# Performance work log

Hardware: AMD Instinct MI355X
Metric: run time of the kernel (lower is better)

## Reference

```python
import jax, jax.numpy as jnp
import numpy as np

B, S, H = 2, 2048, 1024
NH, HD = 16, 64
SCALE = HD ** -0.5


def setup_inputs() -> dict:
    key = jax.random.key(0)
    k1, k2, k3, k4 = jax.random.split(key, 4)
    hidden_states = jax.random.normal(k1, (B, S, H), dtype=jnp.float32)
    attention_mask = jax.random.randint(k2, (B, S), 0, 2, dtype=jnp.int32)
    # xavier-uniform-ish init scale
    w_qkv = jax.random.normal(k3, (3 * H, H), dtype=jnp.float32) * (2.0 / (H + 3 * H)) ** 0.5
    w_out = jax.random.normal(k4, (H, H), dtype=jnp.float32) * (1.0 / H) ** 0.5
    return {"hidden_states": hidden_states, "attention_mask": attention_mask,
            "w_qkv": w_qkv, "w_out": w_out}


def reference(hidden_states, attention_mask, w_qkv, w_out):
    b, s, _ = hidden_states.shape
    qkv = hidden_states @ w_qkv.T                      # [B,S,3H]
    q, k, v = jnp.split(qkv, 3, axis=-1)
    # [B,S,H] -> [B,NH,S,HD]
    reshape = lambda x: x.reshape(b, s, NH, HD).transpose(0, 2, 1, 3)
    q, k, v = reshape(q), reshape(k), reshape(v)
    scores = jnp.einsum('bhqd,bhkd->bhqk', q, k) * SCALE   # [B,NH,S,S]
    mask = attention_mask[:, None, None, :] == 0           # [B,1,1,S]
    scores = jnp.where(mask, -jnp.inf, scores)
    attn = jax.nn.softmax(scores, axis=-1)                 # dropout p: eval mode -> identity
    out = jnp.einsum('bhqk,bhkd->bhqd', attn, v)           # [B,NH,S,HD]
    out = out.transpose(0, 2, 1, 3).reshape(b, s, H)
    return out @ w_out.T
```

## Files before the change

kernel.cpp:

```cpp
#include <hip/hip_runtime.h>
#include <string.h>


typedef __bf16    bf16x8 __attribute__((ext_vector_type(8)));
typedef _Float16  f16x4  __attribute__((ext_vector_type(4)));
typedef _Float16  f16x2  __attribute__((ext_vector_type(2)));
typedef float     f32x4  __attribute__((ext_vector_type(4)));

#define NTOK   4096
#define HDIM   1024
#define SEQ    2048
#define NHEAD  16
#define F2SHIFT 4.0f
#define QSCALE  0.18033688f
#define LSTRIDE 68

__device__ __forceinline__ float bf2f(unsigned short u) {
    union { unsigned int i; float f; } x;
    x.i = ((unsigned int)u) << 16;
    return x.f;
}
__device__ __forceinline__ unsigned short f2bf(float f) {
    union { __bf16 h; unsigned short u; } x;
    x.h = (__bf16)f;
    return x.u;
}
__device__ __forceinline__ unsigned short f2h(float f) {
    union { _Float16 h; unsigned short u; } x;
    x.h = (_Float16)f;
    return x.u;
}
__device__ __forceinline__ f16x2 pkrtz(float a, float b) {
    union { __fp16 __attribute__((ext_vector_type(2))) i; f16x2 o; } x;
    x.i = __builtin_amdgcn_cvt_pkrtz(a, b);
    return x.o;
}

__device__ __forceinline__ int detect_f32(const unsigned short* hs) {
    unsigned int idx = (threadIdx.x & 63) * 4096u;
    float f = bf2f(hs[idx]);
    return __any(!(fabsf(f) < 1e4f));
}

typedef const __attribute__((address_space(1))) unsigned int* gptr_u32;
typedef __attribute__((address_space(3))) unsigned int* lptr_u32;

__device__ __forceinline__ void async16(const unsigned short* g, unsigned short* l) {
    __builtin_amdgcn_global_load_lds((gptr_u32)g, (lptr_u32)l, 16, 0, 0);
}

__global__ void convert3_kernel(const void* __restrict__ s0, const void* __restrict__ s1,
                                const void* __restrict__ s2, unsigned short* __restrict__ dst) {
    const int isf32 = detect_f32((const unsigned short*)s0);
    if (!isf32) return;
    int g = blockIdx.x * blockDim.x + threadIdx.x;
    const int stride = gridDim.x * blockDim.x;
    for (; g < 1048576; g += stride) {
        int i = g * 8;
        const void* src; int off;
        if (i < 4194304)      { src = s0; off = i; }
        else if (i < 7340032) { src = s1; off = i - 4194304; }
        else                  { src = s2; off = i - 7340032; }
        const float* s = (const float*)src + off;
        unsigned short o[8];
#pragma unroll
        for (int j = 0; j < 8; j++) o[j] = f2bf(s[j]);
        *(uint4*)(dst + i) = *(const uint4*)o;
    }
}

__global__ __launch_bounds__(256) void gemm_qkv(
    const unsigned short* __restrict__ Xc, const unsigned short* __restrict__ Wc,
    const unsigned short* __restrict__ Xraw, const unsigned short* __restrict__ Wraw,
    unsigned short* __restrict__ q_out, unsigned short* __restrict__ k_out,
    unsigned short* __restrict__ v_out) {
    const int K = 1024;
    __shared__ __align__(16) unsigned short Xs[128 * 32];
    __shared__ __align__(16) unsigned short Ws[128 * 32];

    const int isf32 = detect_f32(Xraw);
    const unsigned short* X = isf32 ? Xc : Xraw;
    const unsigned short* W = isf32 ? Wc : Wraw;

    const int t = threadIdx.x;
    const int w = t >> 6, lane = t & 63, quad = lane >> 4, lr = lane & 15;
    const int wrow = (w >> 1) * 64, wcol = (w & 1) * 64;
    const int m0 = blockIdx.y * 128, n0 = blockIdx.x * 128;
    const bool vblk = (n0 >= 2048);

    f32x4 acc[4][4];
#pragma unroll
    for (int mi = 0; mi < 4; mi++)
#pragma unroll
        for (int ni = 0; ni < 4; ni++) acc[mi][ni] = (f32x4){0.f, 0.f, 0.f, 0.f};

    const int srow = w * 32 + (lane >> 2);
    const int scol = (lane & 3) * 8;
    const unsigned short* xg = X + (size_t)(m0 + srow) * K + scol;
    const unsigned short* wg = W + (size_t)(n0 + srow) * K + scol;
    unsigned short* xl0 = &Xs[w * 1024];
    unsigned short* wl0 = &Ws[w * 1024];

    for (int k0 = 0; k0 < K; k0 += 32) {
        __syncthreads();
        async16(xg + k0, xl0);
        async16(xg + k0 + 16 * K, xl0 + 512);
        async16(wg + k0, wl0);
        async16(wg + k0 + 16 * K, wl0 + 512);
        __syncthreads();
        bf16x8 af[4], bfr[4];
#pragma unroll
        for (int mi = 0; mi < 4; mi++)
            af[mi] = *(bf16x8*)&Xs[(wrow + mi * 16 + lr) * 32 + quad * 8];
#pragma unroll
        for (int ni = 0; ni < 4; ni++)
            bfr[ni] = *(bf16x8*)&Ws[(wcol + ni * 16 + lr) * 32 + quad * 8];
        if (!vblk) {
#pragma unroll
            for (int mi = 0; mi < 4; mi++)
#pragma unroll
                for (int ni = 0; ni < 4; ni++)
                    acc[mi][ni] = __builtin_amdgcn_mfma_f32_16x16x32_bf16(af[mi], bfr[ni], acc[mi][ni], 0, 0, 0);
        } else {
#pragma unroll
            for (int mi = 0; mi < 4; mi++)
#pragma unroll
                for (int ni = 0; ni < 4; ni++)
                    acc[mi][ni] = __builtin_amdgcn_mfma_f32_16x16x32_bf16(bfr[ni], af[mi], acc[mi][ni], 0, 0, 0);
        }
    }

    if (!vblk) {
#pragma unroll
        for (int mi = 0; mi < 4; mi++)
#pragma unroll
            for (int ni = 0; ni < 4; ni++)
#pragma unroll
                for (int rr = 0; rr < 4; rr++) {
                    int mrow = m0 + wrow + mi * 16 + quad * 4 + rr;
                    int j = n0 + wcol + ni * 16 + lr;
                    float val = acc[mi][ni][rr];
                    int which = j >> 10, rem = j & 1023;
                    int nh = rem >> 6, hd = rem & 63;
                    int b = mrow >> 11, s = mrow & 2047;
                    size_t dst = ((size_t)(b * NHEAD + nh) * SEQ + s) * 64 + hd;
                    if (which == 0) q_out[dst] = f2bf(val * QSCALE);
                    else            k_out[dst] = f2bf(val);
                }
    } else {
#pragma unroll
        for (int mi = 0; mi < 4; mi++)
#pragma unroll
            for (int ni = 0; ni < 4; ni++)
#pragma unroll
                for (int rr = 0; rr < 4; rr++) {
                    int n = n0 + wcol + ni * 16 + quad * 4 + rr;
                    int m = m0 + wrow + mi * 16 + lr;
                    float val = acc[mi][ni][rr];
                    int rem = n & 1023;
                    int nh = rem >> 6, hd = rem & 63;
                    int b = m >> 11, s = m & 2047;
                    size_t dst = ((size_t)(b * NHEAD + nh) * 64 + hd) * SEQ + s;
                    v_out[dst] = f2h(val);
                }
    }
}

__global__ __launch_bounds__(256) void gemm_out(
    const unsigned short* __restrict__ X, const unsigned short* __restrict__ Wc,
    const unsigned short* __restrict__ Wraw,
    void* __restrict__ d_out, const unsigned short* __restrict__ hs_raw) {
    const int K = 1024, N = 1024;
    __shared__ __align__(16) unsigned short Xs[64 * 32];
    __shared__ __align__(16) unsigned short Ws[128 * 32];

    const int isf32 = detect_f32(hs_raw);
    const unsigned short* W = isf32 ? Wc : Wraw;

    const int t = threadIdx.x;
    const int w = t >> 6, lane = t & 63, quad = lane >> 4, lr = lane & 15;
    const int wrow = (w >> 1) * 32, wcol = (w & 1) * 64;
    const int m0 = blockIdx.y * 64, n0 = blockIdx.x * 128;

    f32x4 acc[2][4];
#pragma unroll
    for (int mi = 0; mi < 2; mi++)
#pragma unroll
        for (int ni = 0; ni < 4; ni++) acc[mi][ni] = (f32x4){0.f, 0.f, 0.f, 0.f};

    const int sxrow = w * 16 + (lane >> 2);
    const int swrow = w * 32 + (lane >> 2);
    const int scol = (lane & 3) * 8;
    const unsigned short* xg = X + (size_t)(m0 + sxrow) * K + scol;
    const unsigned short* wg = W + (size_t)(n0 + swrow) * K + scol;
    unsigned short* xl0 = &Xs[w * 512];
    unsigned short* wl0 = &Ws[w * 1024];

    for (int k0 = 0; k0 < K; k0 += 32) {
        __syncthreads();
        async16(xg + k0, xl0);
        async16(wg + k0, wl0);
        async16(wg + k0 + 16 * K, wl0 + 512);
        __syncthreads();
        bf16x8 af[2], bfr[4];
#pragma unroll
        for (int mi = 0; mi < 2; mi++)
            af[mi] = *(bf16x8*)&Xs[(wrow + mi * 16 + lr) * 32 + quad * 8];
#pragma unroll
        for (int ni = 0; ni < 4; ni++)
            bfr[ni] = *(bf16x8*)&Ws[(wcol + ni * 16 + lr) * 32 + quad * 8];
#pragma unroll
        for (int mi = 0; mi < 2; mi++)
#pragma unroll
            for (int ni = 0; ni < 4; ni++)
                acc[mi][ni] = __builtin_amdgcn_mfma_f32_16x16x32_bf16(af[mi], bfr[ni], acc[mi][ni], 0, 0, 0);
    }

#pragma unroll
    for (int mi = 0; mi < 2; mi++)
#pragma unroll
        for (int ni = 0; ni < 4; ni++)
#pragma unroll
            for (int rr = 0; rr < 4; rr++) {
                int mrow = m0 + wrow + mi * 16 + quad * 4 + rr;
                int j = n0 + wcol + ni * 16 + lr;
                float val = acc[mi][ni][rr];
                size_t dst = (size_t)mrow * N + j;
                if (isf32) ((float*)d_out)[dst] = val;
                else ((unsigned short*)d_out)[dst] = f2bf(val);
            }
}

__global__ __launch_bounds__(256) void flash_attn_v7(
    const unsigned short* __restrict__ q, const unsigned short* __restrict__ k,
    const unsigned short* __restrict__ vt, const int* __restrict__ mask,
    unsigned short* __restrict__ attn_out) {
    __shared__ __align__(16) unsigned short Ks[64 * LSTRIDE];
    __shared__ __align__(16) unsigned short Vt[64 * LSTRIDE];
    __shared__ __align__(16) float Msk[80];

    const int t = threadIdx.x;
    const int w = t >> 6, lane = t & 63, quad = lane >> 4, lr = lane & 15;
    const int bh = blockIdx.x, b = bh >> 4, h = bh & 15;
    const int q0 = blockIdx.y * 128;

    const unsigned short* qb = q + (size_t)bh * SEQ * 64;
    const unsigned short* kb = k + (size_t)bh * SEQ * 64;
    const unsigned short* vtb = vt + (size_t)bh * 64 * SEQ;
    const int* mb = mask + b * SEQ;

    bf16x8 qf[2][2];
#pragma unroll
    for (int qg = 0; qg < 2; qg++) {
        const unsigned short* qrow = qb + (size_t)(q0 + w * 32 + qg * 16 + lr) * 64 + quad * 8;
        qf[qg][0] = *(const bf16x8*)qrow;
        qf[qg][1] = *(const bf16x8*)(qrow + 32);
    }

    f32x4 oacc[2][4];
#pragma unroll
    for (int qg = 0; qg < 2; qg++)
#pragma unroll
        for (int dt = 0; dt < 4; dt++) oacc[qg][dt] = (f32x4){0.f, 0.f, 0.f, 0.f};
    float l_st[2] = {0.f, 0.f};

    const int sr = t >> 2;
    const int sc = (t & 3) * 16;

    for (int kk0 = 0; kk0 < SEQ; kk0 += 64) {
        const uint4* kp = (const uint4*)(kb + (size_t)(kk0 + sr) * 64 + sc);
        const uint4* vp = (const uint4*)(vtb + (size_t)sr * SEQ + kk0 + sc);
        uint4 ka = kp[0], kb2 = kp[1];
        uint4 va = vp[0], vb2 = vp[1];
        float mval = 0.f;
        if (t < 64) mval = (mb[kk0 + t] == 0) ? -1e30f : -F2SHIFT;

        __syncthreads();
        *(uint4*)&Ks[sr * LSTRIDE + sc] = ka;
        *(uint4*)&Ks[sr * LSTRIDE + sc + 8] = kb2;
        *(uint4*)&Vt[sr * LSTRIDE + sc] = va;
        *(uint4*)&Vt[sr * LSTRIDE + sc + 8] = vb2;
        if (t < 64) Msk[t] = mval;
        __syncthreads();

#pragma unroll
        for (int mt = 0; mt < 4; mt++) {
            bf16x8 a1h0 = *(bf16x8*)&Ks[(mt * 16 + lr) * LSTRIDE + quad * 8];
            bf16x8 a1h1 = *(bf16x8*)&Ks[(mt * 16 + lr) * LSTRIDE + 32 + quad * 8];
            f16x4 a2[4];
#pragma unroll
            for (int dt = 0; dt < 4; dt++)
                a2[dt] = *(f16x4*)&Vt[(dt * 16 + lr) * LSTRIDE + mt * 16 + quad * 4];
            float4 mv = *(const float4*)&Msk[mt * 16 + quad * 4];

#pragma unroll
            for (int qg = 0; qg < 2; qg++) {
                f32x4 z = (f32x4){0.f, 0.f, 0.f, 0.f};
                z = __builtin_amdgcn_mfma_f32_16x16x32_bf16(a1h0, qf[qg][0], z, 0, 0, 0);
                z = __builtin_amdgcn_mfma_f32_16x16x32_bf16(a1h1, qf[qg][1], z, 0, 0, 0);
                float p0 = __builtin_amdgcn_exp2f(z[0] + mv.x);
                float p1 = __builtin_amdgcn_exp2f(z[1] + mv.y);
                float p2 = __builtin_amdgcn_exp2f(z[2] + mv.z);
                float p3 = __builtin_amdgcn_exp2f(z[3] + mv.w);
                l_st[qg] += (p0 + p1) + (p2 + p3);
                f16x2 ab = pkrtz(p0, p1);
                f16x2 cd = pkrtz(p2, p3);
                f16x4 b2;
                b2[0] = ab[0]; b2[1] = ab[1]; b2[2] = cd[0]; b2[3] = cd[1];
#pragma unroll
                for (int dt = 0; dt < 4; dt++)
                    oacc[qg][dt] = __builtin_amdgcn_mfma_f32_16x16x16f16(a2[dt], b2, oacc[qg][dt], 0, 0, 0);
            }
        }
    }

    float inv[2];
#pragma unroll
    for (int qg = 0; qg < 2; qg++) {
        float s = l_st[qg];
        s += __shfl_xor(s, 16);
        s += __shfl_xor(s, 32);
        inv[qg] = 1.0f / s;
    }
#pragma unroll
    for (int qg = 0; qg < 2; qg++) {
        size_t tok = (size_t)(b * SEQ + q0 + w * 32 + qg * 16 + lr);
#pragma unroll
        for (int dt = 0; dt < 4; dt++)
#pragma unroll
            for (int rr = 0; rr < 4; rr++)
                attn_out[tok * HDIM + h * 64 + dt * 16 + quad * 4 + rr] =
                    f2bf(oacc[qg][dt][rr] * inv[qg]);
    }
}

extern "C" void kernel_launch(void* const* d_in, const int* in_sizes, int n_in,
                              void* d_out, int out_size, void* d_ws, size_t ws_size,
                              hipStream_t stream) {
    const void* hs_raw = d_in[0];
    const int* mask = (const int*)d_in[1];
    const void* wqkv_raw = d_in[2];
    const void* wout_raw = d_in[3];

    char* wsb = (char*)d_ws;
    unsigned short* hs_c = (unsigned short*)(wsb + 256);
    unsigned short* wqkv_c = hs_c + 4194304;
    unsigned short* wout_c = wqkv_c + 3145728;
    unsigned short* qw = wout_c + 1048576;
    unsigned short* kw = qw + 4194304;
    unsigned short* vtw = kw + 4194304;
    unsigned short* ao = vtw + 4194304;

    convert3_kernel<<<1024, 256, 0, stream>>>(hs_raw, wqkv_raw, wout_raw, hs_c);

    gemm_qkv<<<dim3(24, 32), 256, 0, stream>>>(hs_c, wqkv_c,
                                               (const unsigned short*)hs_raw,
                                               (const unsigned short*)wqkv_raw,
                                               qw, kw, vtw);
    flash_attn_v7<<<dim3(32, 16), 256, 0, stream>>>(qw, kw, vtw, mask, ao);
    gemm_out<<<dim3(8, 64), 256, 0, stream>>>(ao, wout_c,
                                              (const unsigned short*)wout_raw, d_out,
                                              (const unsigned short*)hs_raw);
}
```

Measured before the change: 195.0 us.

## Double-buffer K/V tiles in flash attention and fold mask into MFMA accumulator

The attention kernel now keeps two LDS buffers for K, V^T and the mask. The next tile's global loads are issued before computing on the current tile, so memory latency overlaps with the MFMA and exp work. The mask/shift values seed the first QK MFMA accumulator instead of being added after it, removing four adds per group, and s_setprio raises wave priority during the compute section. LDS use doubles, which may reduce occupancy, and the extra live prefetch registers add register pressure.

```diff
diff --git a/kernel.cpp b/kernel.cpp
--- a/kernel.cpp
+++ b/kernel.cpp
@@ -231,13 +231,13 @@
             }
 }
 
-__global__ __launch_bounds__(256) void flash_attn_v7(
+__global__ __launch_bounds__(256) void flash_attn_v8(
     const unsigned short* __restrict__ q, const unsigned short* __restrict__ k,
     const unsigned short* __restrict__ vt, const int* __restrict__ mask,
     unsigned short* __restrict__ attn_out) {
-    __shared__ __align__(16) unsigned short Ks[64 * LSTRIDE];
-    __shared__ __align__(16) unsigned short Vt[64 * LSTRIDE];
-    __shared__ __align__(16) float Msk[80];
+    __shared__ __align__(16) unsigned short Ks[2][64 * LSTRIDE];
+    __shared__ __align__(16) unsigned short Vt[2][64 * LSTRIDE];
+    __shared__ __align__(16) float Msk[2][80];
 
     const int t = threadIdx.x;
     const int w = t >> 6, lane = t & 63, quad = lane >> 4, lr = lane & 15;
@@ -267,41 +267,53 @@
     const int sr = t >> 2;
     const int sc = (t & 3) * 16;
 
+    uint4 ka, kb2, va, vb2;
+    float mval = 0.f;
+    {
+        const uint4* kp = (const uint4*)(kb + (size_t)sr * 64 + sc);
+        const uint4* vp = (const uint4*)(vtb + (size_t)sr * SEQ + sc);
+        ka = kp[0]; kb2 = kp[1];
+        va = vp[0]; vb2 = vp[1];
+        if (t < 64) mval = (mb[t] == 0) ? -1e30f : -F2SHIFT;
+    }
+    *(uint4*)&Ks[0][sr * LSTRIDE + sc] = ka;
+    *(uint4*)&Ks[0][sr * LSTRIDE + sc + 8] = kb2;
+    *(uint4*)&Vt[0][sr * LSTRIDE + sc] = va;
+    *(uint4*)&Vt[0][sr * LSTRIDE + sc + 8] = vb2;
+    if (t < 64) Msk[0][t] = mval;
+    __syncthreads();
+
+    int cur = 0;
     for (int kk0 = 0; kk0 < SEQ; kk0 += 64) {
-        const uint4* kp = (const uint4*)(kb + (size_t)(kk0 + sr) * 64 + sc);
-        const uint4* vp = (const uint4*)(vtb + (size_t)sr * SEQ + kk0 + sc);
-        uint4 ka = kp[0], kb2 = kp[1];
-        uint4 va = vp[0], vb2 = vp[1];
-        float mval = 0.f;
-        if (t < 64) mval = (mb[kk0 + t] == 0) ? -1e30f : -F2SHIFT;
-
-        __syncthreads();
-        *(uint4*)&Ks[sr * LSTRIDE + sc] = ka;
-        *(uint4*)&Ks[sr * LSTRIDE + sc + 8] = kb2;
-        *(uint4*)&Vt[sr * LSTRIDE + sc] = va;
-        *(uint4*)&Vt[sr * LSTRIDE + sc + 8] = vb2;
-        if (t < 64) Msk[t] = mval;
-        __syncthreads();
-
+        const int nxt = kk0 + 64;
+        if (nxt < SEQ) {
+            const uint4* kp = (const uint4*)(kb + (size_t)(nxt + sr) * 64 + sc);
+            const uint4* vp = (const uint4*)(vtb + (size_t)sr * SEQ + nxt + sc);
+            ka = kp[0]; kb2 = kp[1];
+            va = vp[0]; vb2 = vp[1];
+            if (t < 64) mval = (mb[nxt + t] == 0) ? -1e30f : -F2SHIFT;
+        }
+
+        __builtin_amdgcn_s_setprio(1);
 #pragma unroll
         for (int mt = 0; mt < 4; mt++) {
-            bf16x8 a1h0 = *(bf16x8*)&Ks[(mt * 16 + lr) * LSTRIDE + quad * 8];
-            bf16x8 a1h1 = *(bf16x8*)&Ks[(mt * 16 + lr) * LSTRIDE + 32 + quad * 8];
+            bf16x8 a1h0 = *(bf16x8*)&Ks[cur][(mt * 16 + lr) * LSTRIDE + quad * 8];
+            bf16x8 a1h1 = *(bf16x8*)&Ks[cur][(mt * 16 + lr) * LSTRIDE + 32 + quad * 8];
             f16x4 a2[4];
 #pragma unroll
             for (int dt = 0; dt < 4; dt++)
-                a2[dt] = *(f16x4*)&Vt[(dt * 16 + lr) * LSTRIDE + mt * 16 + quad * 4];
-            float4 mv = *(const float4*)&Msk[mt * 16 + quad * 4];
+                a2[dt] = *(f16x4*)&Vt[cur][(dt * 16 + lr) * LSTRIDE + mt * 16 + quad * 4];
+            float4 mv = *(const float4*)&Msk[cur][mt * 16 + quad * 4];
+            f32x4 zi = (f32x4){mv.x, mv.y, mv.z, mv.w};
 
 #pragma unroll
             for (int qg = 0; qg < 2; qg++) {
-                f32x4 z = (f32x4){0.f, 0.f, 0.f, 0.f};
-                z = __builtin_amdgcn_mfma_f32_16x16x32_bf16(a1h0, qf[qg][0], z, 0, 0, 0);
+                f32x4 z = __builtin_amdgcn_mfma_f32_16x16x32_bf16(a1h0, qf[qg][0], zi, 0, 0, 0);
                 z = __builtin_amdgcn_mfma_f32_16x16x32_bf16(a1h1, qf[qg][1], z, 0, 0, 0);
-                float p0 = __builtin_amdgcn_exp2f(z[0] + mv.x);
-                float p1 = __builtin_amdgcn_exp2f(z[1] + mv.y);
-                float p2 = __builtin_amdgcn_exp2f(z[2] + mv.z);
-                float p3 = __builtin_amdgcn_exp2f(z[3] + mv.w);
+                float p0 = __builtin_amdgcn_exp2f(z[0]);
+                float p1 = __builtin_amdgcn_exp2f(z[1]);
+                float p2 = __builtin_amdgcn_exp2f(z[2]);
+                float p3 = __builtin_amdgcn_exp2f(z[3]);
                 l_st[qg] += (p0 + p1) + (p2 + p3);
                 f16x2 ab = pkrtz(p0, p1);
                 f16x2 cd = pkrtz(p2, p3);
@@ -311,6 +323,19 @@
                 for (int dt = 0; dt < 4; dt++)
                     oacc[qg][dt] = __builtin_amdgcn_mfma_f32_16x16x16f16(a2[dt], b2, oacc[qg][dt], 0, 0, 0);
             }
+        }
+        __builtin_amdgcn_s_setprio(0);
+
+        if (nxt < SEQ) {
+            __syncthreads();
+            const int nb = cur ^ 1;
+            *(uint4*)&Ks[nb][sr * LSTRIDE + sc] = ka;
+            *(uint4*)&Ks[nb][sr * LSTRIDE + sc + 8] = kb2;
+            *(uint4*)&Vt[nb][sr * LSTRIDE + sc] = va;
+            *(uint4*)&Vt[nb][sr * LSTRIDE + sc + 8] = vb2;
+            if (t < 64) Msk[nb][t] = mval;
+            __syncthreads();
+            cur = nb;
         }
     }
 
@@ -357,7 +382,7 @@
                                                (const unsigned short*)hs_raw,
                                                (const unsigned short*)wqkv_raw,
                                                qw, kw, vtw);
-    flash_attn_v7<<<dim3(32, 16), 256, 0, stream>>>(qw, kw, vtw, mask, ao);
+    flash_attn_v8<<<dim3(32, 16), 256, 0, stream>>>(qw, kw, vtw, mask, ao);
     gemm_out<<<dim3(8, 64), 256, 0, stream>>>(ao, wout_c,
                                               (const unsigned short*)wout_raw, d_out,
                                               (const unsigned short*)hs_raw);
```

Measured after the change: 202.6 us. +3.9%, slower.

## Read K/V fragments directly from global memory in flash attention, drop LDS staging

Applied to the files above, without the earlier changes.

The attention kernel no longer stages K and V^T tiles through shared memory with two barriers per key block. Each wave loads its MFMA fragments straight from global memory (relying on L1/L2, since all four waves read the same K/V), and the whole mask row is precomputed into LDS once. The mask bias is folded into the MFMA accumulator init instead of being added before exp2, and s_setprio raises wave priority around the compute loop. This removes per-iteration LDS writes and barriers but makes every wave issue redundant global loads with no explicit prefetch, so latency hiding depends on occupancy and cache hits.

```diff
diff --git a/kernel.cpp b/kernel.cpp
--- a/kernel.cpp
+++ b/kernel.cpp
@@ -231,13 +231,11 @@
             }
 }
 
-__global__ __launch_bounds__(256) void flash_attn_v7(
+__global__ __launch_bounds__(256) void flash_attn_v11(
     const unsigned short* __restrict__ q, const unsigned short* __restrict__ k,
     const unsigned short* __restrict__ vt, const int* __restrict__ mask,
     unsigned short* __restrict__ attn_out) {
-    __shared__ __align__(16) unsigned short Ks[64 * LSTRIDE];
-    __shared__ __align__(16) unsigned short Vt[64 * LSTRIDE];
-    __shared__ __align__(16) float Msk[80];
+    __shared__ float Msk[SEQ];
 
     const int t = threadIdx.x;
     const int w = t >> 6, lane = t & 63, quad = lane >> 4, lr = lane & 15;
@@ -249,6 +247,12 @@
     const unsigned short* vtb = vt + (size_t)bh * 64 * SEQ;
     const int* mb = mask + b * SEQ;
 
+#pragma unroll
+    for (int i = 0; i < SEQ / 256; i++) {
+        const int idx = i * 256 + t;
+        Msk[idx] = (mb[idx] == 0) ? -1e30f : -F2SHIFT;
+    }
+
     bf16x8 qf[2][2];
 #pragma unroll
     for (int qg = 0; qg < 2; qg++) {
@@ -264,44 +268,38 @@
         for (int dt = 0; dt < 4; dt++) oacc[qg][dt] = (f32x4){0.f, 0.f, 0.f, 0.f};
     float l_st[2] = {0.f, 0.f};
 
-    const int sr = t >> 2;
-    const int sc = (t & 3) * 16;
+    const unsigned short* kp[4];
+    const unsigned short* vp[4];
+#pragma unroll
+    for (int mt = 0; mt < 4; mt++)
+        kp[mt] = kb + (size_t)(mt * 16 + lr) * 64 + quad * 8;
+#pragma unroll
+    for (int dt = 0; dt < 4; dt++)
+        vp[dt] = vtb + (size_t)(dt * 16 + lr) * SEQ + quad * 4;
+
+    __syncthreads();
 
     for (int kk0 = 0; kk0 < SEQ; kk0 += 64) {
-        const uint4* kp = (const uint4*)(kb + (size_t)(kk0 + sr) * 64 + sc);
-        const uint4* vp = (const uint4*)(vtb + (size_t)sr * SEQ + kk0 + sc);
-        uint4 ka = kp[0], kb2 = kp[1];
-        uint4 va = vp[0], vb2 = vp[1];
-        float mval = 0.f;
-        if (t < 64) mval = (mb[kk0 + t] == 0) ? -1e30f : -F2SHIFT;
-
-        __syncthreads();
-        *(uint4*)&Ks[sr * LSTRIDE + sc] = ka;
-        *(uint4*)&Ks[sr * LSTRIDE + sc + 8] = kb2;
-        *(uint4*)&Vt[sr * LSTRIDE + sc] = va;
-        *(uint4*)&Vt[sr * LSTRIDE + sc + 8] = vb2;
-        if (t < 64) Msk[t] = mval;
-        __syncthreads();
-
+        __builtin_amdgcn_s_setprio(1);
 #pragma unroll
         for (int mt = 0; mt < 4; mt++) {
-            bf16x8 a1h0 = *(bf16x8*)&Ks[(mt * 16 + lr) * LSTRIDE + quad * 8];
-            bf16x8 a1h1 = *(bf16x8*)&Ks[(mt * 16 + lr) * LSTRIDE + 32 + quad * 8];
+            bf16x8 a1h0 = *(const bf16x8*)(kp[mt]);
+            bf16x8 a1h1 = *(const bf16x8*)(kp[mt] + 32);
             f16x4 a2[4];
 #pragma unroll
             for (int dt = 0; dt < 4; dt++)
-                a2[dt] = *(f16x4*)&Vt[(dt * 16 + lr) * LSTRIDE + mt * 16 + quad * 4];
-            float4 mv = *(const float4*)&Msk[mt * 16 + quad * 4];
+                a2[dt] = *(const f16x4*)(vp[dt] + mt * 16);
+            float4 mv = *(const float4*)&Msk[kk0 + mt * 16 + quad * 4];
+            f32x4 zi = (f32x4){mv.x, mv.y, mv.z, mv.w};
 
 #pragma unroll
             for (int qg = 0; qg < 2; qg++) {
-                f32x4 z = (f32x4){0.f, 0.f, 0.f, 0.f};
-                z = __builtin_amdgcn_mfma_f32_16x16x32_bf16(a1h0, qf[qg][0], z, 0, 0, 0);
+                f32x4 z = __builtin_amdgcn_mfma_f32_16x16x32_bf16(a1h0, qf[qg][0], zi, 0, 0, 0);
                 z = __builtin_amdgcn_mfma_f32_16x16x32_bf16(a1h1, qf[qg][1], z, 0, 0, 0);
-                float p0 = __builtin_amdgcn_exp2f(z[0] + mv.x);
-                float p1 = __builtin_amdgcn_exp2f(z[1] + mv.y);
-                float p2 = __builtin_amdgcn_exp2f(z[2] + mv.z);
-                float p3 = __builtin_amdgcn_exp2f(z[3] + mv.w);
+                float p0 = __builtin_amdgcn_exp2f(z[0]);
+                float p1 = __builtin_amdgcn_exp2f(z[1]);
+                float p2 = __builtin_amdgcn_exp2f(z[2]);
+                float p3 = __builtin_amdgcn_exp2f(z[3]);
                 l_st[qg] += (p0 + p1) + (p2 + p3);
                 f16x2 ab = pkrtz(p0, p1);
                 f16x2 cd = pkrtz(p2, p3);
@@ -312,6 +310,12 @@
                     oacc[qg][dt] = __builtin_amdgcn_mfma_f32_16x16x16f16(a2[dt], b2, oacc[qg][dt], 0, 0, 0);
             }
         }
+        __builtin_amdgcn_s_setprio(0);
+
+#pragma unroll
+        for (int mt = 0; mt < 4; mt++) kp[mt] += 64 * 64;
+#pragma unroll
+        for (int dt = 0; dt < 4; dt++) vp[dt] += 64;
     }
 
     float inv[2];
@@ -357,7 +361,7 @@
                                                (const unsigned short*)hs_raw,
                                                (const unsigned short*)wqkv_raw,
                                                qw, kw, vtw);
-    flash_attn_v7<<<dim3(32, 16), 256, 0, stream>>>(qw, kw, vtw, mask, ao);
+    flash_attn_v11<<<dim3(32, 16), 256, 0, stream>>>(qw, kw, vtw, mask, ao);
     gemm_out<<<dim3(8, 64), 256, 0, stream>>>(ao, wout_c,
                                               (const unsigned short*)wout_raw, d_out,
                                               (const unsigned short*)hs_raw);
```

Measured after the change: 319.0 us. 63.6% more time.
